# Optimization experiments

Hardware: AMD Instinct MI355X
Metric: run time of the kernel (lower is better)

The kernel has to match this reference:

```python
import jax, jax.numpy as jnp
import numpy as np


def setup_inputs() -> dict:
    key = jax.random.key(0)
    x = jax.random.normal(key, (512, 2048, 49), dtype=jnp.float32)
    return {"x": x, "k_percent": 90}


def reference(x, k_percent):
    # Per-sample percentile threshold (np.percentile default linear interpolation),
    # then nn.Threshold(th, 0): keep values strictly > th, else 0.
    B = x.shape[0]
    q = k_percent / 100.0
    flat = x.reshape(B, -1)                      # [B, C*HW]
    th = jnp.quantile(flat, q, axis=1)           # [B], linear interpolation (np.percentile default)
    th = th.reshape((B,) + (1,) * (x.ndim - 1))  # broadcast over feature dims
    return jnp.where(x > th, x, jnp.zeros((), dtype=x.dtype))
```

## Files before the change

kernel.cpp:

```cpp
#include <hip/hip_runtime.h>
#include <stdint.h>


constexpr int ROW_LEN      = 2048 * 49;
constexpr int THREADS      = 512;
constexpr int VEC4_PER_ROW = ROW_LEN / 4;
constexpr int ITERS        = VEC4_PER_ROW / THREADS;

__device__ __forceinline__ uint32_t f2s(float f) {
    uint32_t u = __float_as_uint(f);
    return (u & 0x80000000u) ? ~u : (u | 0x80000000u);
}
__device__ __forceinline__ float s2f(uint32_t u) {
    uint32_t b = (u & 0x80000000u) ? (u ^ 0x80000000u) : ~u;
    return __uint_as_float(b);
}

template <int NB>
__device__ void select_bucket(const uint32_t* __restrict__ hist, uint32_t target,
                              uint32_t* sscan, uint32_t* sout) {
    const int tid = threadIdx.x;
    constexpr int CH = NB / THREADS;
    uint32_t s = 0;
#pragma unroll
    for (int j = 0; j < CH; ++j) s += hist[tid * CH + j];
    sscan[tid] = s;
    __syncthreads();
    for (int off = 1; off < THREADS; off <<= 1) {
        uint32_t v = (tid >= off) ? sscan[tid - off] : 0u;
        __syncthreads();
        sscan[tid] += v;
        __syncthreads();
    }
    uint32_t run = sscan[tid] - s;
#pragma unroll
    for (int j = 0; j < CH; ++j) {
        uint32_t c = hist[tid * CH + j];
        if (c != 0u && target >= run && target < run + c) {
            sout[0] = (uint32_t)(tid * CH + j);
            sout[1] = run;
        }
        run += c;
    }
    __syncthreads();
}

__global__ __launch_bounds__(THREADS)
void ash_kernel(const float* __restrict__ x, const int* __restrict__ kp,
                float* __restrict__ out) {
    __shared__ uint32_t h0[2048];
    __shared__ uint32_t h1[2048];
    __shared__ uint32_t sscan[THREADS];
    __shared__ uint32_t sout[4];
    __shared__ float sth;

    const int tid = threadIdx.x;
    const size_t rowoff = (size_t)blockIdx.x * (size_t)ROW_LEN;
    const float4* __restrict__ xr = reinterpret_cast<const float4*>(x + rowoff);

    const int kpv = *kp;
    double q = (double)kpv / 100.0;
    double vidx = q * (double)(ROW_LEN - 1);
    if (vidx < 0.0) vidx = 0.0;
    if (vidx > (double)(ROW_LEN - 1)) vidx = (double)(ROW_LEN - 1);
    uint32_t k0 = (uint32_t)vidx;
    double frac = vidx - (double)k0;
    uint32_t k1 = (k0 + 1u < (uint32_t)ROW_LEN) ? k0 + 1u : k0;

    uint32_t pref0 = 0, pref1 = 0, base0 = 0, base1 = 0;

    for (int i = tid; i < 2048; i += THREADS) h0[i] = 0u;
    __syncthreads();
    for (int it = 0; it < ITERS; ++it) {
        float4 f = xr[it * THREADS + tid];
        atomicAdd(&h0[f2s(f.x) >> 21], 1u);
        atomicAdd(&h0[f2s(f.y) >> 21], 1u);
        atomicAdd(&h0[f2s(f.z) >> 21], 1u);
        atomicAdd(&h0[f2s(f.w) >> 21], 1u);
    }
    __syncthreads();
    select_bucket<2048>(h0, k0, sscan, sout);
    select_bucket<2048>(h0, k1, sscan, sout + 2);
    pref0 = sout[0] << 21; base0 = sout[1];
    pref1 = sout[2] << 21; base1 = sout[3];
    __syncthreads();

    for (int i = tid; i < 2048; i += THREADS) { h0[i] = 0u; h1[i] = 0u; }
    __syncthreads();
    {
        const bool same = (pref0 == pref1);
        const uint32_t p0 = pref0 >> 21, p1 = pref1 >> 21;
        for (int it = 0; it < ITERS; ++it) {
            float4 f = xr[it * THREADS + tid];
            uint32_t u;
            u = f2s(f.x);
            if ((u >> 21) == p0) atomicAdd(&h0[(u >> 10) & 0x7FFu], 1u);
            if (!same && (u >> 21) == p1) atomicAdd(&h1[(u >> 10) & 0x7FFu], 1u);
            u = f2s(f.y);
            if ((u >> 21) == p0) atomicAdd(&h0[(u >> 10) & 0x7FFu], 1u);
            if (!same && (u >> 21) == p1) atomicAdd(&h1[(u >> 10) & 0x7FFu], 1u);
            u = f2s(f.z);
            if ((u >> 21) == p0) atomicAdd(&h0[(u >> 10) & 0x7FFu], 1u);
            if (!same && (u >> 21) == p1) atomicAdd(&h1[(u >> 10) & 0x7FFu], 1u);
            u = f2s(f.w);
            if ((u >> 21) == p0) atomicAdd(&h0[(u >> 10) & 0x7FFu], 1u);
            if (!same && (u >> 21) == p1) atomicAdd(&h1[(u >> 10) & 0x7FFu], 1u);
        }
        __syncthreads();
        select_bucket<2048>(h0, k0 - base0, sscan, sout);
        select_bucket<2048>(same ? h0 : h1, k1 - base1, sscan, sout + 2);
        pref0 |= sout[0] << 10; base0 += sout[1];
        pref1 |= sout[2] << 10; base1 += sout[3];
        __syncthreads();
    }

    for (int i = tid; i < 2048; i += THREADS) { h0[i] = 0u; h1[i] = 0u; }
    __syncthreads();
    {
        const bool same = (pref0 == pref1);
        const uint32_t p0 = pref0 >> 10, p1 = pref1 >> 10;
        for (int it = 0; it < ITERS; ++it) {
            float4 f = xr[it * THREADS + tid];
            uint32_t u;
            u = f2s(f.x);
            if ((u >> 10) == p0) atomicAdd(&h0[u & 0x3FFu], 1u);
            if (!same && (u >> 10) == p1) atomicAdd(&h1[u & 0x3FFu], 1u);
            u = f2s(f.y);
            if ((u >> 10) == p0) atomicAdd(&h0[u & 0x3FFu], 1u);
            if (!same && (u >> 10) == p1) atomicAdd(&h1[u & 0x3FFu], 1u);
            u = f2s(f.z);
            if ((u >> 10) == p0) atomicAdd(&h0[u & 0x3FFu], 1u);
            if (!same && (u >> 10) == p1) atomicAdd(&h1[u & 0x3FFu], 1u);
            u = f2s(f.w);
            if ((u >> 10) == p0) atomicAdd(&h0[u & 0x3FFu], 1u);
            if (!same && (u >> 10) == p1) atomicAdd(&h1[u & 0x3FFu], 1u);
        }
        __syncthreads();
        select_bucket<1024>(h0, k0 - base0, sscan, sout);
        select_bucket<1024>(same ? h0 : h1, k1 - base1, sscan, sout + 2);
        if (tid == 0) {
            uint32_t key0 = pref0 | sout[0];
            uint32_t key1 = pref1 | sout[2];
            double v0 = (double)s2f(key0);
            double v1 = (double)s2f(key1);
            double t = frac;
            double th;
            if (t >= 0.5) th = v1 - (v1 - v0) * (1.0 - t);
            else          th = v0 + (v1 - v0) * t;
            sth = (float)th;
        }
        __syncthreads();
    }

    const float th = sth;
    float4* __restrict__ orow = reinterpret_cast<float4*>(out + rowoff);
    for (int it = 0; it < ITERS; ++it) {
        float4 f = xr[it * THREADS + tid];
        f.x = (f.x > th) ? f.x : 0.0f;
        f.y = (f.y > th) ? f.y : 0.0f;
        f.z = (f.z > th) ? f.z : 0.0f;
        f.w = (f.w > th) ? f.w : 0.0f;
        orow[it * THREADS + tid] = f;
    }
}

extern "C" void kernel_launch(void* const* d_in, const int* in_sizes, int n_in,
                              void* d_out, int out_size, void* d_ws, size_t ws_size,
                              hipStream_t stream) {
    const float* x  = (const float*)d_in[0];
    const int*   kp = (const int*)d_in[1];
    float*       out = (float*)d_out;
    const int rows = in_sizes[0] / ROW_LEN;
    hipLaunchKernelGGL(ash_kernel, dim3(rows), dim3(THREADS), 0, stream,
                       x, kp, out);
}
```

Measured before the change: 435.8 us.

## Compact top-bucket candidates into shared memory to skip global refinement passes

After the first coarse radix histogram pass, the kernel now makes one more pass over the row and compacts every element whose top 11 bits match the target bucket(s) into a shared-memory candidate buffer. The remaining radix refinement, or a min/max reduction when the two order statistics fall in different buckets, runs on that buffer instead of re-reading the row twice from global memory. If the candidates overflow the buffer, it falls back to the old multi-pass path. It also moves to 1024-thread blocks, uses four replicated first-pass histograms to cut LDS atomic contention, and uses nontemporal loads and stores for the final masking pass. The cost is more LDS use per block, which may lower occupancy, plus a single shared counter that all candidate pushes contend on.

```diff
diff --git a/kernel.cpp b/kernel.cpp
--- a/kernel.cpp
+++ b/kernel.cpp
@@ -2,10 +2,14 @@
 #include <stdint.h>
 
 
-constexpr int ROW_LEN      = 2048 * 49;
-constexpr int THREADS      = 512;
-constexpr int VEC4_PER_ROW = ROW_LEN / 4;
-constexpr int ITERS        = VEC4_PER_ROW / THREADS;
+typedef float v4f __attribute__((ext_vector_type(4)));
+
+constexpr int ROW_LEN = 2048 * 49;
+constexpr int THREADS = 1024;
+constexpr int VEC4    = ROW_LEN / 4;
+constexpr int FULL    = VEC4 / THREADS;
+constexpr int TAIL    = VEC4 - FULL * THREADS;
+constexpr int CAP     = 8192;
 
 __device__ __forceinline__ uint32_t f2s(float f) {
     uint32_t u = __float_as_uint(f);
@@ -15,6 +19,8 @@
     uint32_t b = (u & 0x80000000u) ? (u ^ 0x80000000u) : ~u;
     return __uint_as_float(b);
 }
+__device__ __forceinline__ uint32_t umax_(uint32_t a, uint32_t b) { return a > b ? a : b; }
+__device__ __forceinline__ uint32_t umin_(uint32_t a, uint32_t b) { return a < b ? a : b; }
 
 template <int NB>
 __device__ void select_bucket(const uint32_t* __restrict__ hist, uint32_t target,
@@ -45,18 +51,18 @@
     __syncthreads();
 }
 
-__global__ __launch_bounds__(THREADS)
+__global__ __launch_bounds__(THREADS, 8)
 void ash_kernel(const float* __restrict__ x, const int* __restrict__ kp,
                 float* __restrict__ out) {
-    __shared__ uint32_t h0[2048];
-    __shared__ uint32_t h1[2048];
+    __shared__ uint32_t hist[4][2048];
+    __shared__ uint32_t cand[CAP];
     __shared__ uint32_t sscan[THREADS];
     __shared__ uint32_t sout[4];
-    __shared__ float sth;
+    __shared__ uint32_t scnt;
 
     const int tid = threadIdx.x;
     const size_t rowoff = (size_t)blockIdx.x * (size_t)ROW_LEN;
-    const float4* __restrict__ xr = reinterpret_cast<const float4*>(x + rowoff);
+    const v4f* __restrict__ xr = reinterpret_cast<const v4f*>(x + rowoff);
 
     const int kpv = *kp;
     double q = (double)kpv / 100.0;
@@ -67,100 +73,202 @@
     double frac = vidx - (double)k0;
     uint32_t k1 = (k0 + 1u < (uint32_t)ROW_LEN) ? k0 + 1u : k0;
 
-    uint32_t pref0 = 0, pref1 = 0, base0 = 0, base1 = 0;
-
-    for (int i = tid; i < 2048; i += THREADS) h0[i] = 0u;
-    __syncthreads();
-    for (int it = 0; it < ITERS; ++it) {
-        float4 f = xr[it * THREADS + tid];
-        atomicAdd(&h0[f2s(f.x) >> 21], 1u);
-        atomicAdd(&h0[f2s(f.y) >> 21], 1u);
-        atomicAdd(&h0[f2s(f.z) >> 21], 1u);
-        atomicAdd(&h0[f2s(f.w) >> 21], 1u);
-    }
-    __syncthreads();
-    select_bucket<2048>(h0, k0, sscan, sout);
-    select_bucket<2048>(h0, k1, sscan, sout + 2);
-    pref0 = sout[0] << 21; base0 = sout[1];
-    pref1 = sout[2] << 21; base1 = sout[3];
-    __syncthreads();
-
-    for (int i = tid; i < 2048; i += THREADS) { h0[i] = 0u; h1[i] = 0u; }
-    __syncthreads();
     {
-        const bool same = (pref0 == pref1);
-        const uint32_t p0 = pref0 >> 21, p1 = pref1 >> 21;
-        for (int it = 0; it < ITERS; ++it) {
-            float4 f = xr[it * THREADS + tid];
+        uint32_t* hflat = &hist[0][0];
+        for (int i = tid; i < 4 * 2048; i += THREADS) hflat[i] = 0u;
+    }
+    __syncthreads();
+    {
+        uint32_t* hrep = hist[(tid >> 6) & 3];
+#pragma unroll 2
+        for (int it = 0; it < FULL / 2; ++it) {
+            v4f a = xr[(2 * it) * THREADS + tid];
+            v4f b = xr[(2 * it + 1) * THREADS + tid];
+            atomicAdd(&hrep[f2s(a.x) >> 21], 1u);
+            atomicAdd(&hrep[f2s(a.y) >> 21], 1u);
+            atomicAdd(&hrep[f2s(a.z) >> 21], 1u);
+            atomicAdd(&hrep[f2s(a.w) >> 21], 1u);
+            atomicAdd(&hrep[f2s(b.x) >> 21], 1u);
+            atomicAdd(&hrep[f2s(b.y) >> 21], 1u);
+            atomicAdd(&hrep[f2s(b.z) >> 21], 1u);
+            atomicAdd(&hrep[f2s(b.w) >> 21], 1u);
+        }
+        if (tid < TAIL) {
+            v4f a = xr[FULL * THREADS + tid];
+            atomicAdd(&hrep[f2s(a.x) >> 21], 1u);
+            atomicAdd(&hrep[f2s(a.y) >> 21], 1u);
+            atomicAdd(&hrep[f2s(a.z) >> 21], 1u);
+            atomicAdd(&hrep[f2s(a.w) >> 21], 1u);
+        }
+    }
+    __syncthreads();
+    for (int i = tid; i < 2048; i += THREADS)
+        hist[0][i] += hist[1][i] + hist[2][i] + hist[3][i];
+    __syncthreads();
+    select_bucket<2048>(hist[0], k0, sscan, sout);
+    select_bucket<2048>(hist[0], k1, sscan, sout + 2);
+    const uint32_t p0 = sout[0], base0 = sout[1];
+    const uint32_t p1 = sout[2], base1 = sout[3];
+    __syncthreads();
+
+    if (tid == 0) scnt = 0u;
+    __syncthreads();
+    {
+        auto push = [&](uint32_t u) {
+            uint32_t pr = u >> 21;
+            if (pr == p0 || pr == p1) {
+                uint32_t idx = atomicAdd(&scnt, 1u);
+                if (idx < (uint32_t)CAP) cand[idx] = u;
+            }
+        };
+#pragma unroll 2
+        for (int it = 0; it < FULL / 2; ++it) {
+            v4f a = xr[(2 * it) * THREADS + tid];
+            v4f b = xr[(2 * it + 1) * THREADS + tid];
+            push(f2s(a.x)); push(f2s(a.y)); push(f2s(a.z)); push(f2s(a.w));
+            push(f2s(b.x)); push(f2s(b.y)); push(f2s(b.z)); push(f2s(b.w));
+        }
+        if (tid < TAIL) {
+            v4f a = xr[FULL * THREADS + tid];
+            push(f2s(a.x)); push(f2s(a.y)); push(f2s(a.z)); push(f2s(a.w));
+        }
+    }
+    __syncthreads();
+    const uint32_t cnt = scnt;
+
+    uint32_t key0, key1;
+    if (cnt <= (uint32_t)CAP) {
+        if (p0 == p1) {
+            for (int i = tid; i < 2048; i += THREADS) hist[0][i] = 0u;
+            __syncthreads();
+            for (int i = tid; i < (int)cnt; i += THREADS)
+                atomicAdd(&hist[0][(cand[i] >> 10) & 0x7FFu], 1u);
+            __syncthreads();
+            select_bucket<2048>(hist[0], k0 - base0, sscan, sout);
+            select_bucket<2048>(hist[0], k1 - base0, sscan, sout + 2);
+            const uint32_t m0 = sout[0], b0 = sout[1];
+            const uint32_t m1 = sout[2], b1 = sout[3];
+            __syncthreads();
+            for (int i = tid; i < 2048; i += THREADS) { hist[0][i] = 0u; hist[1][i] = 0u; }
+            __syncthreads();
+            for (int i = tid; i < (int)cnt; i += THREADS) {
+                uint32_t u = cand[i];
+                uint32_t m = (u >> 10) & 0x7FFu;
+                if (m == m0) atomicAdd(&hist[0][u & 0x3FFu], 1u);
+                if (m1 != m0 && m == m1) atomicAdd(&hist[1][u & 0x3FFu], 1u);
+            }
+            __syncthreads();
+            select_bucket<1024>(hist[0], (k0 - base0) - b0, sscan, sout);
+            select_bucket<1024>((m1 == m0) ? hist[0] : hist[1], (k1 - base0) - b1,
+                                sscan, sout + 2);
+            key0 = (p0 << 21) | (m0 << 10) | sout[0];
+            key1 = (p0 << 21) | (m1 << 10) | sout[2];
+        } else {
+            uint32_t lmax = 0u, lmin = 0xFFFFFFFFu;
+            for (int i = tid; i < (int)cnt; i += THREADS) {
+                uint32_t u = cand[i];
+                if ((u >> 21) == p0) lmax = umax_(lmax, u);
+                else                 lmin = umin_(lmin, u);
+            }
+            sscan[tid] = lmax;
+            __syncthreads();
+            for (int off = THREADS / 2; off > 0; off >>= 1) {
+                if (tid < off) sscan[tid] = umax_(sscan[tid], sscan[tid + off]);
+                __syncthreads();
+            }
+            key0 = sscan[0];
+            __syncthreads();
+            sscan[tid] = lmin;
+            __syncthreads();
+            for (int off = THREADS / 2; off > 0; off >>= 1) {
+                if (tid < off) sscan[tid] = umin_(sscan[tid], sscan[tid + off]);
+                __syncthreads();
+            }
+            key1 = sscan[0];
+            __syncthreads();
+        }
+    } else {
+        uint32_t bb0 = base0, bb1 = base1;
+        for (int i = tid; i < 2048; i += THREADS) { hist[0][i] = 0u; hist[1][i] = 0u; }
+        __syncthreads();
+        const bool same = (p0 == p1);
+        for (int i = tid; i < VEC4; i += THREADS) {
+            v4f a = xr[i];
             uint32_t u;
-            u = f2s(f.x);
-            if ((u >> 21) == p0) atomicAdd(&h0[(u >> 10) & 0x7FFu], 1u);
-            if (!same && (u >> 21) == p1) atomicAdd(&h1[(u >> 10) & 0x7FFu], 1u);
-            u = f2s(f.y);
-            if ((u >> 21) == p0) atomicAdd(&h0[(u >> 10) & 0x7FFu], 1u);
-            if (!same && (u >> 21) == p1) atomicAdd(&h1[(u >> 10) & 0x7FFu], 1u);
-            u = f2s(f.z);
-            if ((u >> 21) == p0) atomicAdd(&h0[(u >> 10) & 0x7FFu], 1u);
-            if (!same && (u >> 21) == p1) atomicAdd(&h1[(u >> 10) & 0x7FFu], 1u);
-            u = f2s(f.w);
-            if ((u >> 21) == p0) atomicAdd(&h0[(u >> 10) & 0x7FFu], 1u);
-            if (!same && (u >> 21) == p1) atomicAdd(&h1[(u >> 10) & 0x7FFu], 1u);
-        }
-        __syncthreads();
-        select_bucket<2048>(h0, k0 - base0, sscan, sout);
-        select_bucket<2048>(same ? h0 : h1, k1 - base1, sscan, sout + 2);
-        pref0 |= sout[0] << 10; base0 += sout[1];
-        pref1 |= sout[2] << 10; base1 += sout[3];
-        __syncthreads();
-    }
-
-    for (int i = tid; i < 2048; i += THREADS) { h0[i] = 0u; h1[i] = 0u; }
-    __syncthreads();
-    {
-        const bool same = (pref0 == pref1);
-        const uint32_t p0 = pref0 >> 10, p1 = pref1 >> 10;
-        for (int it = 0; it < ITERS; ++it) {
-            float4 f = xr[it * THREADS + tid];
+            u = f2s(a.x);
+            if ((u >> 21) == p0) atomicAdd(&hist[0][(u >> 10) & 0x7FFu], 1u);
+            if (!same && (u >> 21) == p1) atomicAdd(&hist[1][(u >> 10) & 0x7FFu], 1u);
+            u = f2s(a.y);
+            if ((u >> 21) == p0) atomicAdd(&hist[0][(u >> 10) & 0x7FFu], 1u);
+            if (!same && (u >> 21) == p1) atomicAdd(&hist[1][(u >> 10) & 0x7FFu], 1u);
+            u = f2s(a.z);
+            if ((u >> 21) == p0) atomicAdd(&hist[0][(u >> 10) & 0x7FFu], 1u);
+            if (!same && (u >> 21) == p1) atomicAdd(&hist[1][(u >> 10) & 0x7FFu], 1u);
+            u = f2s(a.w);
+            if ((u >> 21) == p0) atomicAdd(&hist[0][(u >> 10) & 0x7FFu], 1u);
+            if (!same && (u >> 21) == p1) atomicAdd(&hist[1][(u >> 10) & 0x7FFu], 1u);
+        }
+        __syncthreads();
+        select_bucket<2048>(hist[0], k0 - bb0, sscan, sout);
+        select_bucket<2048>(same ? hist[0] : hist[1], k1 - bb1, sscan, sout + 2);
+        const uint32_t q0 = (p0 << 11) | sout[0]; bb0 += sout[1];
+        const uint32_t q1 = (p1 << 11) | sout[2]; bb1 += sout[3];
+        __syncthreads();
+        for (int i = tid; i < 2048; i += THREADS) { hist[0][i] = 0u; hist[1][i] = 0u; }
+        __syncthreads();
+        const bool same2 = (q0 == q1);
+        for (int i = tid; i < VEC4; i += THREADS) {
+            v4f a = xr[i];
             uint32_t u;
-            u = f2s(f.x);
-            if ((u >> 10) == p0) atomicAdd(&h0[u & 0x3FFu], 1u);
-            if (!same && (u >> 10) == p1) atomicAdd(&h1[u & 0x3FFu], 1u);
-            u = f2s(f.y);
-            if ((u >> 10) == p0) atomicAdd(&h0[u & 0x3FFu], 1u);
-            if (!same && (u >> 10) == p1) atomicAdd(&h1[u & 0x3FFu], 1u);
-            u = f2s(f.z);
-            if ((u >> 10) == p0) atomicAdd(&h0[u & 0x3FFu], 1u);
-            if (!same && (u >> 10) == p1) atomicAdd(&h1[u & 0x3FFu], 1u);
-            u = f2s(f.w);
-            if ((u >> 10) == p0) atomicAdd(&h0[u & 0x3FFu], 1u);
-            if (!same && (u >> 10) == p1) atomicAdd(&h1[u & 0x3FFu], 1u);
-        }
-        __syncthreads();
-        select_bucket<1024>(h0, k0 - base0, sscan, sout);
-        select_bucket<1024>(same ? h0 : h1, k1 - base1, sscan, sout + 2);
-        if (tid == 0) {
-            uint32_t key0 = pref0 | sout[0];
-            uint32_t key1 = pref1 | sout[2];
-            double v0 = (double)s2f(key0);
-            double v1 = (double)s2f(key1);
-            double t = frac;
-            double th;
-            if (t >= 0.5) th = v1 - (v1 - v0) * (1.0 - t);
-            else          th = v0 + (v1 - v0) * t;
-            sth = (float)th;
-        }
-        __syncthreads();
-    }
-
-    const float th = sth;
-    float4* __restrict__ orow = reinterpret_cast<float4*>(out + rowoff);
-    for (int it = 0; it < ITERS; ++it) {
-        float4 f = xr[it * THREADS + tid];
-        f.x = (f.x > th) ? f.x : 0.0f;
-        f.y = (f.y > th) ? f.y : 0.0f;
-        f.z = (f.z > th) ? f.z : 0.0f;
-        f.w = (f.w > th) ? f.w : 0.0f;
-        orow[it * THREADS + tid] = f;
+            u = f2s(a.x);
+            if ((u >> 10) == q0) atomicAdd(&hist[0][u & 0x3FFu], 1u);
+            if (!same2 && (u >> 10) == q1) atomicAdd(&hist[1][u & 0x3FFu], 1u);
+            u = f2s(a.y);
+            if ((u >> 10) == q0) atomicAdd(&hist[0][u & 0x3FFu], 1u);
+            if (!same2 && (u >> 10) == q1) atomicAdd(&hist[1][u & 0x3FFu], 1u);
+            u = f2s(a.z);
+            if ((u >> 10) == q0) atomicAdd(&hist[0][u & 0x3FFu], 1u);
+            if (!same2 && (u >> 10) == q1) atomicAdd(&hist[1][u & 0x3FFu], 1u);
+            u = f2s(a.w);
+            if ((u >> 10) == q0) atomicAdd(&hist[0][u & 0x3FFu], 1u);
+            if (!same2 && (u >> 10) == q1) atomicAdd(&hist[1][u & 0x3FFu], 1u);
+        }
+        __syncthreads();
+        select_bucket<1024>(hist[0], k0 - bb0, sscan, sout);
+        select_bucket<1024>(same2 ? hist[0] : hist[1], k1 - bb1, sscan, sout + 2);
+        key0 = (q0 << 10) | sout[0];
+        key1 = (q1 << 10) | sout[2];
+    }
+
+    double v0 = (double)s2f(key0);
+    double v1 = (double)s2f(key1);
+    double th_d = (frac >= 0.5) ? v1 - (v1 - v0) * (1.0 - frac)
+                                : v0 + (v1 - v0) * frac;
+    const float th = (float)th_d;
+
+    v4f* __restrict__ orow = reinterpret_cast<v4f*>(out + rowoff);
+#pragma unroll 2
+    for (int it = 0; it < FULL / 2; ++it) {
+        v4f a = __builtin_nontemporal_load(&xr[(2 * it) * THREADS + tid]);
+        v4f b = __builtin_nontemporal_load(&xr[(2 * it + 1) * THREADS + tid]);
+        a.x = (a.x > th) ? a.x : 0.0f;
+        a.y = (a.y > th) ? a.y : 0.0f;
+        a.z = (a.z > th) ? a.z : 0.0f;
+        a.w = (a.w > th) ? a.w : 0.0f;
+        b.x = (b.x > th) ? b.x : 0.0f;
+        b.y = (b.y > th) ? b.y : 0.0f;
+        b.z = (b.z > th) ? b.z : 0.0f;
+        b.w = (b.w > th) ? b.w : 0.0f;
+        __builtin_nontemporal_store(a, &orow[(2 * it) * THREADS + tid]);
+        __builtin_nontemporal_store(b, &orow[(2 * it + 1) * THREADS + tid]);
+    }
+    if (tid < TAIL) {
+        v4f a = __builtin_nontemporal_load(&xr[FULL * THREADS + tid]);
+        a.x = (a.x > th) ? a.x : 0.0f;
+        a.y = (a.y > th) ? a.y : 0.0f;
+        a.z = (a.z > th) ? a.z : 0.0f;
+        a.w = (a.w > th) ? a.w : 0.0f;
+        __builtin_nontemporal_store(a, &orow[FULL * THREADS + tid]);
     }
 }
 
```

New measurement: 391.2 us. 10.2% less time.

## Keep row in registers, privatize first-pass histogram, use wave-shuffle scans

Applied to the files above, without the earlier changes.

Each thread now loads its 49 float4 chunks of the row into registers once with nontemporal loads and reuses them across all three radix passes and the final threshold write, where it previously reread global memory four times. The first-pass histogram is split into four per-wave-group copies to reduce LDS atomic contention, and these are summed afterwards. The prefix scan in bucket selection uses wavefront shuffles plus a small per-wave sum array in place of a barrier-heavy shared-memory scan. Every thread computes the threshold itself and the output uses nontemporal stores. The cost is very high register pressure (196 VGPRs' worth of data per thread), which may cause spilling or lower occupancy.

```diff
diff --git a/kernel.cpp b/kernel.cpp
--- a/kernel.cpp
+++ b/kernel.cpp
@@ -2,10 +2,12 @@
 #include <stdint.h>
 
 
-constexpr int ROW_LEN      = 2048 * 49;
-constexpr int THREADS      = 512;
-constexpr int VEC4_PER_ROW = ROW_LEN / 4;
-constexpr int ITERS        = VEC4_PER_ROW / THREADS;
+typedef float v4f __attribute__((ext_vector_type(4)));
+
+constexpr int ROW_LEN = 2048 * 49;
+constexpr int THREADS = 512;
+constexpr int VEC4    = ROW_LEN / 4;
+constexpr int PER     = VEC4 / THREADS;
 
 __device__ __forceinline__ uint32_t f2s(float f) {
     uint32_t u = __float_as_uint(f);
@@ -17,46 +19,50 @@
 }
 
 template <int NB>
-__device__ void select_bucket(const uint32_t* __restrict__ hist, uint32_t target,
-                              uint32_t* sscan, uint32_t* sout) {
-    const int tid = threadIdx.x;
+__device__ __forceinline__ void select_bucket(const uint32_t* __restrict__ hist,
+                                              uint32_t target,
+                                              uint32_t* wsum, uint32_t* sout) {
+    const int tid  = threadIdx.x;
+    const int lane = tid & 63;
+    const int wid  = tid >> 6;
     constexpr int CH = NB / THREADS;
+    uint32_t c[CH];
     uint32_t s = 0;
 #pragma unroll
-    for (int j = 0; j < CH; ++j) s += hist[tid * CH + j];
-    sscan[tid] = s;
+    for (int j = 0; j < CH; ++j) { c[j] = hist[tid * CH + j]; s += c[j]; }
+    uint32_t inc = s;
+#pragma unroll
+    for (int d = 1; d < 64; d <<= 1) {
+        uint32_t v = __shfl_up(inc, d, 64);
+        if (lane >= d) inc += v;
+    }
+    if (lane == 63) wsum[wid] = inc;
     __syncthreads();
-    for (int off = 1; off < THREADS; off <<= 1) {
-        uint32_t v = (tid >= off) ? sscan[tid - off] : 0u;
-        __syncthreads();
-        sscan[tid] += v;
-        __syncthreads();
-    }
-    uint32_t run = sscan[tid] - s;
+    uint32_t off = 0;
+#pragma unroll
+    for (int w = 0; w < 8; ++w) off += (w < wid) ? wsum[w] : 0u;
+    uint32_t run = off + inc - s;
 #pragma unroll
     for (int j = 0; j < CH; ++j) {
-        uint32_t c = hist[tid * CH + j];
-        if (c != 0u && target >= run && target < run + c) {
+        if (c[j] != 0u && target >= run && target < run + c[j]) {
             sout[0] = (uint32_t)(tid * CH + j);
             sout[1] = run;
         }
-        run += c;
+        run += c[j];
     }
     __syncthreads();
 }
 
-__global__ __launch_bounds__(THREADS)
+__global__ __launch_bounds__(THREADS, 2)
 void ash_kernel(const float* __restrict__ x, const int* __restrict__ kp,
                 float* __restrict__ out) {
-    __shared__ uint32_t h0[2048];
-    __shared__ uint32_t h1[2048];
-    __shared__ uint32_t sscan[THREADS];
+    __shared__ uint32_t hist[4][2048];
+    __shared__ uint32_t wsum[8];
     __shared__ uint32_t sout[4];
-    __shared__ float sth;
 
     const int tid = threadIdx.x;
     const size_t rowoff = (size_t)blockIdx.x * (size_t)ROW_LEN;
-    const float4* __restrict__ xr = reinterpret_cast<const float4*>(x + rowoff);
+    const v4f* __restrict__ xr = reinterpret_cast<const v4f*>(x + rowoff);
 
     const int kpv = *kp;
     double q = (double)kpv / 100.0;
@@ -67,100 +73,108 @@
     double frac = vidx - (double)k0;
     uint32_t k1 = (k0 + 1u < (uint32_t)ROW_LEN) ? k0 + 1u : k0;
 
-    uint32_t pref0 = 0, pref1 = 0, base0 = 0, base1 = 0;
+    v4f d[PER];
+#pragma unroll
+    for (int i = 0; i < PER; ++i)
+        d[i] = __builtin_nontemporal_load(&xr[i * THREADS + tid]);
 
-    for (int i = tid; i < 2048; i += THREADS) h0[i] = 0u;
-    __syncthreads();
-    for (int it = 0; it < ITERS; ++it) {
-        float4 f = xr[it * THREADS + tid];
-        atomicAdd(&h0[f2s(f.x) >> 21], 1u);
-        atomicAdd(&h0[f2s(f.y) >> 21], 1u);
-        atomicAdd(&h0[f2s(f.z) >> 21], 1u);
-        atomicAdd(&h0[f2s(f.w) >> 21], 1u);
+    {
+        uint32_t* hf = &hist[0][0];
+        for (int i = tid; i < 4 * 2048; i += THREADS) hf[i] = 0u;
     }
     __syncthreads();
-    select_bucket<2048>(h0, k0, sscan, sout);
-    select_bucket<2048>(h0, k1, sscan, sout + 2);
-    pref0 = sout[0] << 21; base0 = sout[1];
-    pref1 = sout[2] << 21; base1 = sout[3];
+    {
+        uint32_t* hr = hist[(tid >> 7) & 3];
+#pragma unroll
+        for (int i = 0; i < PER; ++i) {
+            atomicAdd(&hr[f2s(d[i].x) >> 21], 1u);
+            atomicAdd(&hr[f2s(d[i].y) >> 21], 1u);
+            atomicAdd(&hr[f2s(d[i].z) >> 21], 1u);
+            atomicAdd(&hr[f2s(d[i].w) >> 21], 1u);
+        }
+    }
+    __syncthreads();
+    for (int i = tid; i < 2048; i += THREADS)
+        hist[0][i] += hist[1][i] + hist[2][i] + hist[3][i];
+    __syncthreads();
+    select_bucket<2048>(hist[0], k0, wsum, sout);
+    select_bucket<2048>(hist[0], k1, wsum, sout + 2);
+    const uint32_t p0 = sout[0]; uint32_t base0 = sout[1];
+    const uint32_t p1 = sout[2]; uint32_t base1 = sout[3];
     __syncthreads();
 
-    for (int i = tid; i < 2048; i += THREADS) { h0[i] = 0u; h1[i] = 0u; }
+    for (int i = tid; i < 2048; i += THREADS) { hist[0][i] = 0u; hist[1][i] = 0u; }
     __syncthreads();
     {
-        const bool same = (pref0 == pref1);
-        const uint32_t p0 = pref0 >> 21, p1 = pref1 >> 21;
-        for (int it = 0; it < ITERS; ++it) {
-            float4 f = xr[it * THREADS + tid];
+        const bool same1 = (p0 == p1);
+#pragma unroll
+        for (int i = 0; i < PER; ++i) {
             uint32_t u;
-            u = f2s(f.x);
-            if ((u >> 21) == p0) atomicAdd(&h0[(u >> 10) & 0x7FFu], 1u);
-            if (!same && (u >> 21) == p1) atomicAdd(&h1[(u >> 10) & 0x7FFu], 1u);
-            u = f2s(f.y);
-            if ((u >> 21) == p0) atomicAdd(&h0[(u >> 10) & 0x7FFu], 1u);
-            if (!same && (u >> 21) == p1) atomicAdd(&h1[(u >> 10) & 0x7FFu], 1u);
-            u = f2s(f.z);
-            if ((u >> 21) == p0) atomicAdd(&h0[(u >> 10) & 0x7FFu], 1u);
-            if (!same && (u >> 21) == p1) atomicAdd(&h1[(u >> 10) & 0x7FFu], 1u);
-            u = f2s(f.w);
-            if ((u >> 21) == p0) atomicAdd(&h0[(u >> 10) & 0x7FFu], 1u);
-            if (!same && (u >> 21) == p1) atomicAdd(&h1[(u >> 10) & 0x7FFu], 1u);
+            u = f2s(d[i].x);
+            if ((u >> 21) == p0) atomicAdd(&hist[0][(u >> 10) & 0x7FFu], 1u);
+            else if (!same1 && (u >> 21) == p1) atomicAdd(&hist[1][(u >> 10) & 0x7FFu], 1u);
+            u = f2s(d[i].y);
+            if ((u >> 21) == p0) atomicAdd(&hist[0][(u >> 10) & 0x7FFu], 1u);
+            else if (!same1 && (u >> 21) == p1) atomicAdd(&hist[1][(u >> 10) & 0x7FFu], 1u);
+            u = f2s(d[i].z);
+            if ((u >> 21) == p0) atomicAdd(&hist[0][(u >> 10) & 0x7FFu], 1u);
+            else if (!same1 && (u >> 21) == p1) atomicAdd(&hist[1][(u >> 10) & 0x7FFu], 1u);
+            u = f2s(d[i].w);
+            if ((u >> 21) == p0) atomicAdd(&hist[0][(u >> 10) & 0x7FFu], 1u);
+            else if (!same1 && (u >> 21) == p1) atomicAdd(&hist[1][(u >> 10) & 0x7FFu], 1u);
         }
         __syncthreads();
-        select_bucket<2048>(h0, k0 - base0, sscan, sout);
-        select_bucket<2048>(same ? h0 : h1, k1 - base1, sscan, sout + 2);
-        pref0 |= sout[0] << 10; base0 += sout[1];
-        pref1 |= sout[2] << 10; base1 += sout[3];
-        __syncthreads();
+        select_bucket<2048>(hist[0], k0 - base0, wsum, sout);
+        select_bucket<2048>(same1 ? hist[0] : hist[1], k1 - base1, wsum, sout + 2);
     }
+    const uint32_t m0 = sout[0]; base0 += sout[1];
+    const uint32_t m1 = sout[2]; base1 += sout[3];
+    const uint32_t q0 = (p0 << 11) | m0;
+    const uint32_t q1 = (p1 << 11) | m1;
+    __syncthreads();
 
-    for (int i = tid; i < 2048; i += THREADS) { h0[i] = 0u; h1[i] = 0u; }
+    for (int i = tid; i < 2048; i += THREADS) { hist[0][i] = 0u; hist[1][i] = 0u; }
     __syncthreads();
     {
-        const bool same = (pref0 == pref1);
-        const uint32_t p0 = pref0 >> 10, p1 = pref1 >> 10;
-        for (int it = 0; it < ITERS; ++it) {
-            float4 f = xr[it * THREADS + tid];
+        const bool same2 = (q0 == q1);
+#pragma unroll
+        for (int i = 0; i < PER; ++i) {
             uint32_t u;
-            u = f2s(f.x);
-            if ((u >> 10) == p0) atomicAdd(&h0[u & 0x3FFu], 1u);
-            if (!same && (u >> 10) == p1) atomicAdd(&h1[u & 0x3FFu], 1u);
-            u = f2s(f.y);
-            if ((u >> 10) == p0) atomicAdd(&h0[u & 0x3FFu], 1u);
-            if (!same && (u >> 10) == p1) atomicAdd(&h1[u & 0x3FFu], 1u);
-            u = f2s(f.z);
-            if ((u >> 10) == p0) atomicAdd(&h0[u & 0x3FFu], 1u);
-            if (!same && (u >> 10) == p1) atomicAdd(&h1[u & 0x3FFu], 1u);
-            u = f2s(f.w);
-            if ((u >> 10) == p0) atomicAdd(&h0[u & 0x3FFu], 1u);
-            if (!same && (u >> 10) == p1) atomicAdd(&h1[u & 0x3FFu], 1u);
+            u = f2s(d[i].x);
+            if ((u >> 10) == q0) atomicAdd(&hist[0][u & 0x3FFu], 1u);
+            else if (!same2 && (u >> 10) == q1) atomicAdd(&hist[1][u & 0x3FFu], 1u);
+            u = f2s(d[i].y);
+            if ((u >> 10) == q0) atomicAdd(&hist[0][u & 0x3FFu], 1u);
+            else if (!same2 && (u >> 10) == q1) atomicAdd(&hist[1][u & 0x3FFu], 1u);
+            u = f2s(d[i].z);
+            if ((u >> 10) == q0) atomicAdd(&hist[0][u & 0x3FFu], 1u);
+            else if (!same2 && (u >> 10) == q1) atomicAdd(&hist[1][u & 0x3FFu], 1u);
+            u = f2s(d[i].w);
+            if ((u >> 10) == q0) atomicAdd(&hist[0][u & 0x3FFu], 1u);
+            else if (!same2 && (u >> 10) == q1) atomicAdd(&hist[1][u & 0x3FFu], 1u);
         }
         __syncthreads();
-        select_bucket<1024>(h0, k0 - base0, sscan, sout);
-        select_bucket<1024>(same ? h0 : h1, k1 - base1, sscan, sout + 2);
-        if (tid == 0) {
-            uint32_t key0 = pref0 | sout[0];
-            uint32_t key1 = pref1 | sout[2];
-            double v0 = (double)s2f(key0);
-            double v1 = (double)s2f(key1);
-            double t = frac;
-            double th;
-            if (t >= 0.5) th = v1 - (v1 - v0) * (1.0 - t);
-            else          th = v0 + (v1 - v0) * t;
-            sth = (float)th;
-        }
-        __syncthreads();
+        select_bucket<1024>(hist[0], k0 - base0, wsum, sout);
+        select_bucket<1024>(same2 ? hist[0] : hist[1], k1 - base1, wsum, sout + 2);
     }
+    const uint32_t key0 = (q0 << 10) | sout[0];
+    const uint32_t key1 = (q1 << 10) | sout[2];
 
-    const float th = sth;
-    float4* __restrict__ orow = reinterpret_cast<float4*>(out + rowoff);
-    for (int it = 0; it < ITERS; ++it) {
-        float4 f = xr[it * THREADS + tid];
-        f.x = (f.x > th) ? f.x : 0.0f;
-        f.y = (f.y > th) ? f.y : 0.0f;
-        f.z = (f.z > th) ? f.z : 0.0f;
-        f.w = (f.w > th) ? f.w : 0.0f;
-        orow[it * THREADS + tid] = f;
+    double v0 = (double)s2f(key0);
+    double v1 = (double)s2f(key1);
+    double th_d = (frac >= 0.5) ? v1 - (v1 - v0) * (1.0 - frac)
+                                : v0 + (v1 - v0) * frac;
+    const float th = (float)th_d;
+
+    v4f* __restrict__ orow = reinterpret_cast<v4f*>(out + rowoff);
+#pragma unroll
+    for (int i = 0; i < PER; ++i) {
+        v4f a = d[i], r;
+        r.x = (a.x > th) ? a.x : 0.0f;
+        r.y = (a.y > th) ? a.y : 0.0f;
+        r.z = (a.z > th) ? a.z : 0.0f;
+        r.w = (a.w > th) ? a.w : 0.0f;
+        __builtin_nontemporal_store(r, &orow[i * THREADS + tid]);
     }
 }
 
```

Measured after the change: 982.4 us. 125% more time.
